# Kernel optimization log

Measured on AMD Instinct MI355X. Metric: run time of the kernel, lower is better.

## Reference

```python
import jax, jax.numpy as jnp
import numpy as np
import math

B, T, C, V = 64, 4096, 3, 16
HEADS = 4
ROT_HIDDEN = 128
MLP_HIDDEN = 256
NUM_CLASSES = 12
BLOCK_SIZES = (16, 32, 64)
IN_FEAT = C * V  # 48
FEAT_DIM = HEADS * 7 * len(BLOCK_SIZES)  # 84


def _linear_params(key, fan_in, fan_out):
    kw, kb = jax.random.split(key)
    lim = 1.0 / np.sqrt(fan_in)
    w = jax.random.uniform(kw, (fan_in, fan_out), jnp.float32, -lim, lim)
    b = jax.random.uniform(kb, (fan_out,), jnp.float32, -lim, lim)
    return w, b


def setup_inputs() -> dict:
    key = jax.random.key(0)
    ks = jax.random.split(key, 7)
    x = jax.random.normal(ks[0], (B, T, C, V), jnp.float32)
    w1, b1 = _linear_params(ks[1], IN_FEAT, ROT_HIDDEN)
    w2, b2 = _linear_params(ks[2], ROT_HIDDEN, ROT_HIDDEN)
    w3, b3 = _linear_params(ks[3], ROT_HIDDEN, HEADS * 4)
    p1, pb1 = _linear_params(ks[4], FEAT_DIM, MLP_HIDDEN)
    p2, pb2 = _linear_params(ks[5], MLP_HIDDEN, MLP_HIDDEN)
    p3, pb3 = _linear_params(ks[6], MLP_HIDDEN, NUM_CLASSES)
    return dict(x=x, w1=w1, b1=b1, w2=w2, b2=b2, w3=w3, b3=b3,
                p1=p1, pb1=pb1, p2=p2, pb2=pb2, p3=p3, pb3=pb3)


def _extract_tsf(rot, bs):
    # rot: (B, H, T, F). Non-overlapping blocks of size bs (T % bs == 0).
    b, h, t, f = rot.shape
    n = t // bs
    z = rot.reshape(b, h, n, bs, f)
    mean = z.mean(axis=3)
    m2 = (z * z).mean(axis=3)
    std = jnp.sqrt(((z - mean[:, :, :, None, :]) ** 2).mean(axis=3))
    z_min = z.min(axis=3)
    z_max = z.max(axis=3)
    rms = jnp.sqrt(m2 + 1e-8)
    mac = jnp.abs(z[:, :, :, 1:, :] - z[:, :, :, :-1, :]).mean(axis=3)
    energy = m2  # (z**2).sum / bs == mean of squares
    feat = jnp.stack([mean, std, z_min, z_max, rms, mac, energy], axis=-1)  # (B,H,n,F,7)
    # mean over blocks (n) then over channels (F) -> (B, H, 7)
    return feat.mean(axis=2).mean(axis=2)


def reference(x, w1, b1, w2, b2, w3, b3, p1, pb1, p2, pb2, p3, pb3):
    b, t, c, v = x.shape
    xf = x.reshape(b, t, c * v)
    f = xf.shape[-1]
    pad = (3 - f % 3) % 3
    if pad > 0:
        xf = jnp.pad(xf, ((0, 0), (0, 0), (0, pad)))
    g = xf.shape[-1] // 3
    x_xyz = xf.reshape(b, t, g, 3)

    # rotation-parameter MLP (dropout is identity in eval mode)
    gf = xf.mean(axis=1)[:, :IN_FEAT]
    h1 = jax.nn.relu(gf @ w1 + b1)
    h2 = jax.nn.relu(h1 @ w2 + b2)
    rot = jnp.tanh(h2 @ w3 + b3).reshape(b, HEADS, 4)
    axis = rot[..., :3]
    axis = axis / (jnp.linalg.norm(axis, axis=-1, keepdims=True) + 1e-8)
    theta = rot[..., 3] * math.pi  # (B, H)

    # Rodrigues rotation: v (B,1,T,g,3), k (B,H,1,1,3)
    vvec = x_xyz[:, None]
    k = axis[:, :, None, None, :]
    th = theta[:, :, None, None, None]
    cos_t, sin_t = jnp.cos(th), jnp.sin(th)
    cross = jnp.cross(jnp.broadcast_to(k, (b, HEADS, t, g, 3)),
                      jnp.broadcast_to(vvec, (b, HEADS, t, g, 3)), axis=-1)
    dot = (k * vvec).sum(axis=-1, keepdims=True)
    rotated = vvec * cos_t + cross * sin_t + k * dot * (1.0 - cos_t)  # (B,H,T,g,3)
    rotated = rotated.reshape(b, HEADS, t, g * 3)

    # block-wise stats: per head, per block size, 7 stats -> (B, H, nbs, 7)
    feats = jnp.stack([_extract_tsf(rotated, bs) for bs in BLOCK_SIZES], axis=2)
    feat = feats.reshape(b, HEADS * len(BLOCK_SIZES) * 7)  # (B, 84)

    q1 = jax.nn.relu(feat @ p1 + pb1)
    q2 = jax.nn.relu(q1 @ p2 + pb2)
    return q2 @ p3 + pb3
```

## Files before the change

kernel.cpp:

```cpp
#include <hip/hip_runtime.h>
#include <math.h>


#define PI_F 3.14159265358979323846f

__global__ __launch_bounds__(384) void k_colmean(const float4* __restrict__ x4,
                                                 float* __restrict__ gfpart) {
    int b = blockIdx.x >> 3;
    int chunk = blockIdx.x & 7;
    int tid = threadIdx.x;
    int j4 = tid % 12, r = tid / 12;
    const float4* p = x4 + ((size_t)(b * 4096 + chunk * 512 + r)) * 12 + j4;
    float4 s = make_float4(0.f, 0.f, 0.f, 0.f);
#pragma unroll
    for (int i = 0; i < 16; ++i) {
        float4 v = p[(size_t)i * 32 * 12];
        s.x += v.x; s.y += v.y; s.z += v.z; s.w += v.w;
    }
    __shared__ float4 red[384];
    red[tid] = s;
    __syncthreads();
    if (tid < 48) {
        int jj = tid >> 2, c = tid & 3;
        float t = 0.f;
#pragma unroll
        for (int rr = 0; rr < 32; ++rr) {
            const float* q = (const float*)&red[rr * 12 + jj];
            t += q[c];
        }
        gfpart[blockIdx.x * 48 + tid] = t;
    }
}

__global__ __launch_bounds__(128) void k_rot(const float* __restrict__ gfpart,
                                             const float* __restrict__ w1, const float* __restrict__ b1,
                                             const float* __restrict__ w2, const float* __restrict__ b2,
                                             const float* __restrict__ w3, const float* __restrict__ b3,
                                             float* __restrict__ Rmat) {
    int b = blockIdx.x;
    int j = threadIdx.x;
    __shared__ float gf_s[48], h1_s[128], h2_s[128], rot_s[16];
    if (j < 48) {
        float s = 0.f;
#pragma unroll
        for (int ch = 0; ch < 8; ++ch) s += gfpart[(b * 8 + ch) * 48 + j];
        gf_s[j] = s * (1.f / 4096.f);
    }
    __syncthreads();
    float a = b1[j];
#pragma unroll
    for (int i = 0; i < 48; ++i) a = fmaf(gf_s[i], w1[i * 128 + j], a);
    h1_s[j] = fmaxf(a, 0.f);
    __syncthreads();
    a = b2[j];
    for (int i = 0; i < 128; ++i) a = fmaf(h1_s[i], w2[i * 128 + j], a);
    h2_s[j] = fmaxf(a, 0.f);
    __syncthreads();
    if (j < 16) {
        a = b3[j];
        for (int i = 0; i < 128; ++i) a = fmaf(h2_s[i], w3[i * 16 + j], a);
        rot_s[j] = tanhf(a);
    }
    __syncthreads();
    if (j < 4) {
        float kx = rot_s[j * 4 + 0], ky = rot_s[j * 4 + 1], kz = rot_s[j * 4 + 2];
        float w = rot_s[j * 4 + 3];
        float nrm = sqrtf(kx * kx + ky * ky + kz * kz) + 1e-8f;
        kx /= nrm; ky /= nrm; kz /= nrm;
        float th = w * PI_F;
        float c = cosf(th), s = sinf(th), C = 1.f - c;
        float* R = Rmat + ((size_t)b * 4 + j) * 9;
        R[0] = c + kx * kx * C;      R[1] = kx * ky * C - kz * s; R[2] = kx * kz * C + ky * s;
        R[3] = ky * kx * C + kz * s; R[4] = c + ky * ky * C;      R[5] = ky * kz * C - kx * s;
        R[6] = kz * kx * C - ky * s; R[7] = kz * ky * C + kx * s; R[8] = c + kz * kz * C;
    }
}

__global__ __launch_bounds__(256) void k_stats(const float* __restrict__ x,
                                               const float* __restrict__ Rmat,
                                               float* __restrict__ accpart) {
    __shared__ float xs[256 * 48];
    int bid = blockIdx.x;
    int b = bid >> 4;
    int tile = bid & 15;
    int tid = threadIdx.x;

    {
        const float4* src = (const float4*)(x + ((size_t)b * 4096 + (size_t)tile * 256) * 48);
        float4* dst = (float4*)xs;
#pragma unroll
        for (int i = 0; i < 12; ++i) dst[tid + 256 * i] = src[tid + 256 * i];
    }

    int grp = tid >> 6;
    int lane = tid & 63;
    int g = lane & 15;
    int h = lane >> 4;

    const float* Rp = Rmat + ((size_t)(b * 4 + h)) * 9;
    float R0 = Rp[0], R1 = Rp[1], R2 = Rp[2];
    float R3 = Rp[3], R4 = Rp[4], R5 = Rp[5];
    float R6 = Rp[6], R7 = Rp[7], R8 = Rp[8];

    __syncthreads();

    const float* rowp = xs + (grp * 64) * 48 + 3 * g;

    float a21[21];
#pragma unroll
    for (int i = 0; i < 21; ++i) a21[i] = 0.f;

    float p32s[3] = {0, 0, 0}, p32q[3] = {0, 0, 0}, p32n[3], p32x[3], p32m[3] = {0, 0, 0};
    float p64s[3] = {0, 0, 0}, p64q[3] = {0, 0, 0}, p64n[3], p64x[3], p64m[3] = {0, 0, 0};
#pragma unroll
    for (int c = 0; c < 3; ++c) { p32n[c] = 1e30f; p32x[c] = -1e30f; p64n[c] = 1e30f; p64x[c] = -1e30f; }
    float prev[3];

#pragma unroll
    for (int k = 0; k < 4; ++k) {
        float cs[3], cq[3], cn[3], cx[3], cm[3];
        {
            const float* p = rowp + (k * 16) * 48;
            float v0 = p[0], v1 = p[1], v2 = p[2];
            float yy[3];
            yy[0] = R0 * v0 + R1 * v1 + R2 * v2;
            yy[1] = R3 * v0 + R4 * v1 + R5 * v2;
            yy[2] = R6 * v0 + R7 * v1 + R8 * v2;
#pragma unroll
            for (int c = 0; c < 3; ++c) {
                float y = yy[c];
                if (k > 0) {
                    float bd = fabsf(y - prev[c]);
                    if (k != 2) p32m[c] += bd;
                    p64m[c] += bd;
                }
                cs[c] = y; cq[c] = y * y; cn[c] = y; cx[c] = y; cm[c] = 0.f; prev[c] = y;
            }
        }
#pragma unroll
        for (int t = 1; t < 16; ++t) {
            const float* p = rowp + (k * 16 + t) * 48;
            float v0 = p[0], v1 = p[1], v2 = p[2];
            float yy[3];
            yy[0] = R0 * v0 + R1 * v1 + R2 * v2;
            yy[1] = R3 * v0 + R4 * v1 + R5 * v2;
            yy[2] = R6 * v0 + R7 * v1 + R8 * v2;
#pragma unroll
            for (int c = 0; c < 3; ++c) {
                float y = yy[c];
                cs[c] += y;
                cq[c] = fmaf(y, y, cq[c]);
                cn[c] = fminf(cn[c], y);
                cx[c] = fmaxf(cx[c], y);
                cm[c] += fabsf(y - prev[c]);
                prev[c] = y;
            }
        }
#pragma unroll
        for (int c = 0; c < 3; ++c) {
            float mean = cs[c] * (1.f / 16.f);
            float m2 = cq[c] * (1.f / 16.f);
            a21[0] += cs[c];
            a21[1] += sqrtf(fmaxf(m2 - mean * mean, 0.f));
            a21[2] += cn[c];
            a21[3] += cx[c];
            a21[4] += sqrtf(m2 + 1e-8f);
            a21[5] += cm[c];
            a21[6] += cq[c];
            p32s[c] += cs[c]; p32q[c] += cq[c];
            p32n[c] = fminf(p32n[c], cn[c]); p32x[c] = fmaxf(p32x[c], cx[c]); p32m[c] += cm[c];
        }
        if (k & 1) {
#pragma unroll
            for (int c = 0; c < 3; ++c) {
                float mean = p32s[c] * (1.f / 32.f);
                float m2 = p32q[c] * (1.f / 32.f);
                a21[7] += p32s[c];
                a21[8] += sqrtf(fmaxf(m2 - mean * mean, 0.f));
                a21[9] += p32n[c];
                a21[10] += p32x[c];
                a21[11] += sqrtf(m2 + 1e-8f);
                a21[12] += p32m[c];
                a21[13] += p32q[c];
                p64s[c] += p32s[c]; p64q[c] += p32q[c];
                p64n[c] = fminf(p64n[c], p32n[c]); p64x[c] = fmaxf(p64x[c], p32x[c]); p64m[c] += p32m[c];
                p32s[c] = 0.f; p32q[c] = 0.f; p32n[c] = 1e30f; p32x[c] = -1e30f; p32m[c] = 0.f;
            }
        }
    }
#pragma unroll
    for (int c = 0; c < 3; ++c) {
        float mean = p64s[c] * (1.f / 64.f);
        float m2 = p64q[c] * (1.f / 64.f);
        a21[14] += p64s[c];
        a21[15] += sqrtf(fmaxf(m2 - mean * mean, 0.f));
        a21[16] += p64n[c];
        a21[17] += p64x[c];
        a21[18] += sqrtf(m2 + 1e-8f);
        a21[19] += p64m[c];
        a21[20] += p64q[c];
    }

    __syncthreads();
    float* red = xs;
#pragma unroll
    for (int q = 0; q < 21; ++q) red[tid * 21 + q] = a21[q];
    __syncthreads();
    if (tid < 84) {
        int hh = tid / 21, sq = tid % 21;
        float s = 0.f;
        for (int u = 0; u < 64; ++u) {
            int src_t = (u >> 4) * 64 + hh * 16 + (u & 15);
            s += red[src_t * 21 + sq];
        }
        accpart[bid * 84 + tid] = s;
    }
}

__global__ __launch_bounds__(256) void k_head(const float* __restrict__ accpart,
                                              const float* __restrict__ p1, const float* __restrict__ pb1,
                                              const float* __restrict__ p2, const float* __restrict__ pb2,
                                              const float* __restrict__ p3, const float* __restrict__ pb3,
                                              float* __restrict__ out) {
    int b = blockIdx.x, j = threadIdx.x;
    __shared__ float feat_s[84], q1_s[256], q2_s[256];
    if (j < 84) {
        float raw = 0.f;
#pragma unroll
        for (int t = 0; t < 16; ++t) raw += accpart[(b * 16 + t) * 84 + j];
        int s = (j % 21) / 7;
        int q = j % 7;
        float bs = (float)(16 << s);
        float n = 4096.f / bs;
        float base = n * 48.f;
        float divi;
        if (q == 0 || q == 6) divi = base * bs;
        else if (q == 5) divi = base * (bs - 1.f);
        else divi = base;
        feat_s[j] = raw / divi;
    }
    __syncthreads();
    float a = pb1[j];
#pragma unroll
    for (int i = 0; i < 84; ++i) a = fmaf(feat_s[i], p1[i * 256 + j], a);
    q1_s[j] = fmaxf(a, 0.f);
    __syncthreads();
    a = pb2[j];
    for (int i = 0; i < 256; ++i) a = fmaf(q1_s[i], p2[i * 256 + j], a);
    q2_s[j] = fmaxf(a, 0.f);
    __syncthreads();
    if (j < 12) {
        a = pb3[j];
        for (int i = 0; i < 256; ++i) a = fmaf(q2_s[i], p3[i * 12 + j], a);
        out[b * 12 + j] = a;
    }
}

extern "C" void kernel_launch(void* const* d_in, const int* in_sizes, int n_in,
                              void* d_out, int out_size, void* d_ws, size_t ws_size,
                              hipStream_t stream) {
    const float* x  = (const float*)d_in[0];
    const float* w1 = (const float*)d_in[1];
    const float* b1 = (const float*)d_in[2];
    const float* w2 = (const float*)d_in[3];
    const float* b2 = (const float*)d_in[4];
    const float* w3 = (const float*)d_in[5];
    const float* b3 = (const float*)d_in[6];
    const float* p1 = (const float*)d_in[7];
    const float* pb1 = (const float*)d_in[8];
    const float* p2 = (const float*)d_in[9];
    const float* pb2 = (const float*)d_in[10];
    const float* p3 = (const float*)d_in[11];
    const float* pb3 = (const float*)d_in[12];

    float* ws = (float*)d_ws;
    float* gfpart  = ws;
    float* Rmat    = ws + 24576;
    float* accpart = ws + 26880;

    k_colmean<<<512, 384, 0, stream>>>((const float4*)x, gfpart);
    k_rot<<<64, 128, 0, stream>>>(gfpart, w1, b1, w2, b2, w3, b3, Rmat);
    k_stats<<<1024, 256, 0, stream>>>(x, Rmat, accpart);
    k_head<<<64, 256, 0, stream>>>(accpart, p1, pb1, p2, pb2, p3, pb3, (float*)d_out);
}
```

Baseline: 63.58 us.

## Fuse rotation MLP into stats kernel, read x directly, shuffle-reduce partials

Removes the separate k_rot launch. Every stats block now recomputes the small rotation MLP (48→128→128→16) for its batch and keeps the rotation matrices in shared memory. The 48KB shared-memory staging of the x tile is replaced by direct strided global loads, and the per-thread 21-value reduction uses wavefront xor shuffles instead of a large shared buffer. This cuts a launch and shared-memory pressure, which may raise occupancy, but adds the MLP work to each of 1024 blocks (16x redundant) and uses uncoalesced 12-byte global reads.

```diff
diff --git a/kernel.cpp b/kernel.cpp
--- a/kernel.cpp
+++ b/kernel.cpp
@@ -32,79 +32,69 @@
     }
 }
 
-__global__ __launch_bounds__(128) void k_rot(const float* __restrict__ gfpart,
-                                             const float* __restrict__ w1, const float* __restrict__ b1,
-                                             const float* __restrict__ w2, const float* __restrict__ b2,
-                                             const float* __restrict__ w3, const float* __restrict__ b3,
-                                             float* __restrict__ Rmat) {
-    int b = blockIdx.x;
-    int j = threadIdx.x;
+__global__ __launch_bounds__(256) void k_stats(const float* __restrict__ x,
+                                               const float* __restrict__ gfpart,
+                                               const float* __restrict__ w1, const float* __restrict__ b1,
+                                               const float* __restrict__ w2, const float* __restrict__ b2,
+                                               const float* __restrict__ w3, const float* __restrict__ b3,
+                                               float* __restrict__ accpart) {
+    int bid = blockIdx.x;
+    int b = bid >> 4;
+    int tile = bid & 15;
+    int tid = threadIdx.x;
+
     __shared__ float gf_s[48], h1_s[128], h2_s[128], rot_s[16];
-    if (j < 48) {
+    __shared__ float Rs[4][9];
+    if (tid < 48) {
         float s = 0.f;
 #pragma unroll
-        for (int ch = 0; ch < 8; ++ch) s += gfpart[(b * 8 + ch) * 48 + j];
-        gf_s[j] = s * (1.f / 4096.f);
-    }
-    __syncthreads();
-    float a = b1[j];
-#pragma unroll
-    for (int i = 0; i < 48; ++i) a = fmaf(gf_s[i], w1[i * 128 + j], a);
-    h1_s[j] = fmaxf(a, 0.f);
-    __syncthreads();
-    a = b2[j];
-    for (int i = 0; i < 128; ++i) a = fmaf(h1_s[i], w2[i * 128 + j], a);
-    h2_s[j] = fmaxf(a, 0.f);
-    __syncthreads();
-    if (j < 16) {
-        a = b3[j];
-        for (int i = 0; i < 128; ++i) a = fmaf(h2_s[i], w3[i * 16 + j], a);
-        rot_s[j] = tanhf(a);
-    }
-    __syncthreads();
-    if (j < 4) {
-        float kx = rot_s[j * 4 + 0], ky = rot_s[j * 4 + 1], kz = rot_s[j * 4 + 2];
-        float w = rot_s[j * 4 + 3];
+        for (int ch = 0; ch < 8; ++ch) s += gfpart[(b * 8 + ch) * 48 + tid];
+        gf_s[tid] = s * (1.f / 4096.f);
+    }
+    __syncthreads();
+    if (tid < 128) {
+        float a = b1[tid];
+#pragma unroll
+        for (int i = 0; i < 48; ++i) a = fmaf(gf_s[i], w1[i * 128 + tid], a);
+        h1_s[tid] = fmaxf(a, 0.f);
+    }
+    __syncthreads();
+    if (tid < 128) {
+        float a = b2[tid];
+        for (int i = 0; i < 128; ++i) a = fmaf(h1_s[i], w2[i * 128 + tid], a);
+        h2_s[tid] = fmaxf(a, 0.f);
+    }
+    __syncthreads();
+    if (tid < 16) {
+        float a = b3[tid];
+        for (int i = 0; i < 128; ++i) a = fmaf(h2_s[i], w3[i * 16 + tid], a);
+        rot_s[tid] = tanhf(a);
+    }
+    __syncthreads();
+    if (tid < 4) {
+        float kx = rot_s[tid * 4 + 0], ky = rot_s[tid * 4 + 1], kz = rot_s[tid * 4 + 2];
+        float w = rot_s[tid * 4 + 3];
         float nrm = sqrtf(kx * kx + ky * ky + kz * kz) + 1e-8f;
         kx /= nrm; ky /= nrm; kz /= nrm;
         float th = w * PI_F;
         float c = cosf(th), s = sinf(th), C = 1.f - c;
-        float* R = Rmat + ((size_t)b * 4 + j) * 9;
+        float* R = &Rs[tid][0];
         R[0] = c + kx * kx * C;      R[1] = kx * ky * C - kz * s; R[2] = kx * kz * C + ky * s;
         R[3] = ky * kx * C + kz * s; R[4] = c + ky * ky * C;      R[5] = ky * kz * C - kx * s;
         R[6] = kz * kx * C - ky * s; R[7] = kz * ky * C + kx * s; R[8] = c + kz * kz * C;
     }
-}
-
-__global__ __launch_bounds__(256) void k_stats(const float* __restrict__ x,
-                                               const float* __restrict__ Rmat,
-                                               float* __restrict__ accpart) {
-    __shared__ float xs[256 * 48];
-    int bid = blockIdx.x;
-    int b = bid >> 4;
-    int tile = bid & 15;
-    int tid = threadIdx.x;
-
-    {
-        const float4* src = (const float4*)(x + ((size_t)b * 4096 + (size_t)tile * 256) * 48);
-        float4* dst = (float4*)xs;
-#pragma unroll
-        for (int i = 0; i < 12; ++i) dst[tid + 256 * i] = src[tid + 256 * i];
-    }
+    __syncthreads();
 
     int grp = tid >> 6;
     int lane = tid & 63;
     int g = lane & 15;
     int h = lane >> 4;
 
-    const float* Rp = Rmat + ((size_t)(b * 4 + h)) * 9;
-    float R0 = Rp[0], R1 = Rp[1], R2 = Rp[2];
-    float R3 = Rp[3], R4 = Rp[4], R5 = Rp[5];
-    float R6 = Rp[6], R7 = Rp[7], R8 = Rp[8];
-
-    __syncthreads();
-
-    const float* rowp = xs + (grp * 64) * 48 + 3 * g;
+    float R0 = Rs[h][0], R1 = Rs[h][1], R2 = Rs[h][2];
+    float R3 = Rs[h][3], R4 = Rs[h][4], R5 = Rs[h][5];
+    float R6 = Rs[h][6], R7 = Rs[h][7], R8 = Rs[h][8];
+
+    const float* rowp = x + ((size_t)(b * 4096 + tile * 256 + grp * 64)) * 48 + 3 * g;
 
     float a21[21];
 #pragma unroll
@@ -120,7 +110,7 @@
     for (int k = 0; k < 4; ++k) {
         float cs[3], cq[3], cn[3], cx[3], cm[3];
         {
-            const float* p = rowp + (k * 16) * 48;
+            const float* p = rowp + (size_t)(k * 16) * 48;
             float v0 = p[0], v1 = p[1], v2 = p[2];
             float yy[3];
             yy[0] = R0 * v0 + R1 * v1 + R2 * v2;
@@ -139,7 +129,7 @@
         }
 #pragma unroll
         for (int t = 1; t < 16; ++t) {
-            const float* p = rowp + (k * 16 + t) * 48;
+            const float* p = rowp + (size_t)(k * 16 + t) * 48;
             float v0 = p[0], v1 = p[1], v2 = p[2];
             float yy[3];
             yy[0] = R0 * v0 + R1 * v1 + R2 * v2;
@@ -201,19 +191,21 @@
         a21[20] += p64q[c];
     }
 
-    __syncthreads();
-    float* red = xs;
-#pragma unroll
-    for (int q = 0; q < 21; ++q) red[tid * 21 + q] = a21[q];
+#pragma unroll
+    for (int m = 1; m <= 8; m <<= 1) {
+#pragma unroll
+        for (int q = 0; q < 21; ++q) a21[q] += __shfl_xor(a21[q], m);
+    }
+    __shared__ float red[4][4][21];
+    if (g == 0) {
+#pragma unroll
+        for (int q = 0; q < 21; ++q) red[grp][h][q] = a21[q];
+    }
     __syncthreads();
     if (tid < 84) {
         int hh = tid / 21, sq = tid % 21;
-        float s = 0.f;
-        for (int u = 0; u < 64; ++u) {
-            int src_t = (u >> 4) * 64 + hh * 16 + (u & 15);
-            s += red[src_t * 21 + sq];
-        }
-        accpart[bid * 84 + tid] = s;
+        accpart[bid * 84 + tid] =
+            red[0][hh][sq] + red[1][hh][sq] + red[2][hh][sq] + red[3][hh][sq];
     }
 }
 
@@ -275,11 +267,9 @@
 
     float* ws = (float*)d_ws;
     float* gfpart  = ws;
-    float* Rmat    = ws + 24576;
-    float* accpart = ws + 26880;
+    float* accpart = ws + 24576;
 
     k_colmean<<<512, 384, 0, stream>>>((const float4*)x, gfpart);
-    k_rot<<<64, 128, 0, stream>>>(gfpart, w1, b1, w2, b2, w3, b3, Rmat);
-    k_stats<<<1024, 256, 0, stream>>>(x, Rmat, accpart);
+    k_stats<<<1024, 256, 0, stream>>>(x, gfpart, w1, b1, w2, b2, w3, b3, accpart);
     k_head<<<64, 256, 0, stream>>>(accpart, p1, pb1, p2, pb2, p3, pb3, (float*)d_out);
 }
```

Result: slower. 92.54 us (+45.6%).

## Load x directly into registers with wave shuffles instead of staging in LDS

Applied to the files above, without the earlier changes.

The stats kernel no longer copies a 48KB tile of x into shared memory. Each lane loads three floats straight from global memory, and the four heads' lanes exchange them with wave shuffles. The final reduction now uses butterfly shuffles within each wave and a small 4x4x21 shared array, replacing the large LDS scratch and the serial 64-element loop. This aims to raise occupancy (launch bounds 256,4) and cut LDS traffic and barriers, at the cost of many more shuffle instructions and strided, poorly coalesced global loads.

```diff
diff --git a/kernel.cpp b/kernel.cpp
--- a/kernel.cpp
+++ b/kernel.cpp
@@ -76,35 +76,25 @@
     }
 }
 
-__global__ __launch_bounds__(256) void k_stats(const float* __restrict__ x,
-                                               const float* __restrict__ Rmat,
-                                               float* __restrict__ accpart) {
-    __shared__ float xs[256 * 48];
+__global__ __launch_bounds__(256, 4) void k_stats(const float* __restrict__ x,
+                                                  const float* __restrict__ Rmat,
+                                                  float* __restrict__ accpart) {
     int bid = blockIdx.x;
     int b = bid >> 4;
     int tile = bid & 15;
     int tid = threadIdx.x;
-
-    {
-        const float4* src = (const float4*)(x + ((size_t)b * 4096 + (size_t)tile * 256) * 48);
-        float4* dst = (float4*)xs;
-#pragma unroll
-        for (int i = 0; i < 12; ++i) dst[tid + 256 * i] = src[tid + 256 * i];
-    }
-
-    int grp = tid >> 6;
+    int w = tid >> 6;
     int lane = tid & 63;
     int g = lane & 15;
     int h = lane >> 4;
 
-    const float* Rp = Rmat + ((size_t)(b * 4 + h)) * 9;
+    const float* Rp = Rmat + (size_t)(b * 4 + h) * 9;
     float R0 = Rp[0], R1 = Rp[1], R2 = Rp[2];
     float R3 = Rp[3], R4 = Rp[4], R5 = Rp[5];
     float R6 = Rp[6], R7 = Rp[7], R8 = Rp[8];
 
-    __syncthreads();
-
-    const float* rowp = xs + (grp * 64) * 48 + 3 * g;
+    const float* lp0 = x + ((size_t)(b * 4096 + tile * 256 + w * 64) + (lane >> 4)) * 48
+                         + 3 * (lane & 15);
 
     float a21[21];
 #pragma unroll
@@ -115,45 +105,47 @@
 #pragma unroll
     for (int c = 0; c < 3; ++c) { p32n[c] = 1e30f; p32x[c] = -1e30f; p64n[c] = 1e30f; p64x[c] = -1e30f; }
     float prev[3];
+    float cs[3], cq[3], cn[3], cx[3], cm[3];
 
 #pragma unroll
     for (int k = 0; k < 4; ++k) {
-        float cs[3], cq[3], cn[3], cx[3], cm[3];
-        {
-            const float* p = rowp + (k * 16) * 48;
-            float v0 = p[0], v1 = p[1], v2 = p[2];
-            float yy[3];
-            yy[0] = R0 * v0 + R1 * v1 + R2 * v2;
-            yy[1] = R3 * v0 + R4 * v1 + R5 * v2;
-            yy[2] = R6 * v0 + R7 * v1 + R8 * v2;
-#pragma unroll
-            for (int c = 0; c < 3; ++c) {
-                float y = yy[c];
-                if (k > 0) {
-                    float bd = fabsf(y - prev[c]);
-                    if (k != 2) p32m[c] += bd;
-                    p64m[c] += bd;
+#pragma unroll
+        for (int tq = 0; tq < 4; ++tq) {
+            const float* lp = lp0 + (size_t)(k * 16 + tq * 4) * 48;
+            float v0 = lp[0], v1 = lp[1], v2 = lp[2];
+#pragma unroll
+            for (int j = 0; j < 4; ++j) {
+                int srcl = (j << 4) | g;
+                float u0 = __shfl(v0, srcl, 64);
+                float u1 = __shfl(v1, srcl, 64);
+                float u2 = __shfl(v2, srcl, 64);
+                float yy[3];
+                yy[0] = fmaf(R0, u0, fmaf(R1, u1, R2 * u2));
+                yy[1] = fmaf(R3, u0, fmaf(R4, u1, R5 * u2));
+                yy[2] = fmaf(R6, u0, fmaf(R7, u1, R8 * u2));
+                if (tq == 0 && j == 0) {
+#pragma unroll
+                    for (int c = 0; c < 3; ++c) {
+                        float y = yy[c];
+                        if (k > 0) {
+                            float bd = fabsf(y - prev[c]);
+                            if (k != 2) p32m[c] += bd;
+                            p64m[c] += bd;
+                        }
+                        cs[c] = y; cq[c] = y * y; cn[c] = y; cx[c] = y; cm[c] = 0.f; prev[c] = y;
+                    }
+                } else {
+#pragma unroll
+                    for (int c = 0; c < 3; ++c) {
+                        float y = yy[c];
+                        cs[c] += y;
+                        cq[c] = fmaf(y, y, cq[c]);
+                        cn[c] = fminf(cn[c], y);
+                        cx[c] = fmaxf(cx[c], y);
+                        cm[c] += fabsf(y - prev[c]);
+                        prev[c] = y;
+                    }
                 }
-                cs[c] = y; cq[c] = y * y; cn[c] = y; cx[c] = y; cm[c] = 0.f; prev[c] = y;
-            }
-        }
-#pragma unroll
-        for (int t = 1; t < 16; ++t) {
-            const float* p = rowp + (k * 16 + t) * 48;
-            float v0 = p[0], v1 = p[1], v2 = p[2];
-            float yy[3];
-            yy[0] = R0 * v0 + R1 * v1 + R2 * v2;
-            yy[1] = R3 * v0 + R4 * v1 + R5 * v2;
-            yy[2] = R6 * v0 + R7 * v1 + R8 * v2;
-#pragma unroll
-            for (int c = 0; c < 3; ++c) {
-                float y = yy[c];
-                cs[c] += y;
-                cq[c] = fmaf(y, y, cq[c]);
-                cn[c] = fminf(cn[c], y);
-                cx[c] = fmaxf(cx[c], y);
-                cm[c] += fabsf(y - prev[c]);
-                prev[c] = y;
             }
         }
 #pragma unroll
@@ -201,19 +193,21 @@
         a21[20] += p64q[c];
     }
 
-    __syncthreads();
-    float* red = xs;
-#pragma unroll
-    for (int q = 0; q < 21; ++q) red[tid * 21 + q] = a21[q];
+#pragma unroll
+    for (int m = 1; m <= 8; m <<= 1) {
+#pragma unroll
+        for (int q = 0; q < 21; ++q) a21[q] += __shfl_xor(a21[q], m);
+    }
+    __shared__ float red[4][4][21];
+    if (g == 0) {
+#pragma unroll
+        for (int q = 0; q < 21; ++q) red[w][h][q] = a21[q];
+    }
     __syncthreads();
     if (tid < 84) {
         int hh = tid / 21, sq = tid % 21;
-        float s = 0.f;
-        for (int u = 0; u < 64; ++u) {
-            int src_t = (u >> 4) * 64 + hh * 16 + (u & 15);
-            s += red[src_t * 21 + sq];
-        }
-        accpart[bid * 84 + tid] = s;
+        accpart[bid * 84 + tid] =
+            red[0][hh][sq] + red[1][hh][sq] + red[2][hh][sq] + red[3][hh][sq];
     }
 }
 
```

Result: slower. 121.8 us (+91.6%).
